# Performance work log

Measured on AMD Instinct MI355X. Metric: run time of the kernel, lower is better.

The kernel has to match this reference:

```python
import jax, jax.numpy as jnp
import numpy as np
import math

EPS = 0.1
N_ITER = 200
SCALE = 1.0
ATOL = 1e-4
RTOL = 1e-4
THRESH = 100.0
D = 2
LOGZ = math.log((2.0 * math.pi * EPS) ** (D / 2.0))


def setup_inputs() -> dict:
    key = jax.random.key(0)
    k1, k2 = jax.random.split(key)
    n, m = 4096, 4096
    # points scaled so C/eps stays O(1) -> K well within fp32 range
    x_spt = 0.3 * jax.random.normal(k1, (n, D), dtype=jnp.float32)
    y_spt = 0.3 * jax.random.normal(k2, (m, D), dtype=jnp.float32)
    x_w = jnp.ones((n,), jnp.float32) / n
    y_w = jnp.ones((m,), jnp.float32) / m
    return {"x_w": x_w, "x_spt": x_spt, "y_w": y_w, "y_spt": y_spt}


def _cdist2(x, y):
    # squared euclidean distance matrix [n, m] via gemm form
    x2 = jnp.sum(x * x, axis=1)
    y2 = jnp.sum(y * y, axis=1)
    d2 = x2[:, None] + y2[None, :] - 2.0 * (x @ y.T)
    return jnp.maximum(d2, 0.0)


def _getK(C, x_w, y_w, a, b):
    return jnp.exp(-(C + a[:, None] + b[None, :]) / EPS - LOGZ) * x_w[:, None] * y_w[None, :]


def _sinkhorn(C, x_w, y_w):
    # balanced Sinkhorn fixed point with absorption/stabilization, mirrors torch loop
    n, m = C.shape
    u0 = jnp.ones((n,), C.dtype)
    v0 = jnp.ones((m,), C.dtype)
    a0 = jnp.zeros((n,), C.dtype)
    b0 = jnp.zeros((m,), C.dtype)
    K0 = _getK(C, x_w, y_w, a0, b0)
    yw_norm = jnp.max(jnp.abs(y_w))

    def cond(st):
        i, u, v, a, b, K, done = st
        return (i < N_ITER) & (~done)

    def body(st):
        i, u, v, a, b, K, done = st
        v = y_w / (K.T @ u)      # proxdiv_balanced
        u = x_w / (K @ v)
        err = jnp.max(jnp.abs(v * (K.T @ u) - y_w))
        done = (err < ATOL) | (err / yw_norm < RTOL)
        stab = (jnp.maximum(jnp.max(jnp.abs(u)), jnp.max(jnp.abs(v))) > THRESH) & (~done)

        def do_stab(ops):
            u_, v_, a_, b_, K_ = ops
            a2 = a_ - EPS * jnp.log(u_)
            b2 = b_ - EPS * jnp.log(v_)
            return (jnp.ones_like(u_), jnp.ones_like(v_), a2, b2, _getK(C, x_w, y_w, a2, b2))

        u, v, a, b, K = jax.lax.cond(stab, do_stab, lambda ops: ops, (u, v, a, b, K))
        return (i + 1, u, v, a, b, K, done)

    st = jax.lax.while_loop(cond, body, (jnp.int32(0), u0, v0, a0, b0, K0, jnp.bool_(False)))
    return st[1], st[2], st[3], st[4]


def _obj_dual(C, x_w, y_w, u, v, a, b):
    f = -EPS * jnp.log(u) + a
    g = -EPS * jnp.log(v) + b
    f_cts = EPS * jax.nn.logsumexp((-C - g[None, :]) / EPS + jnp.log(y_w)[None, :], axis=1) - EPS * LOGZ
    g_cts = EPS * jax.nn.logsumexp((-C - f[:, None]) / EPS + jnp.log(x_w)[:, None], axis=0) - EPS * LOGZ
    f1 = f_cts @ x_w   # F_indicator_star (balanced)
    f2 = g_cts @ y_w
    plan = jnp.exp(-(C + f_cts[:, None] + g_cts[None, :]) / EPS - LOGZ) * x_w[:, None] * y_w[None, :]
    return -f1 - f2 - EPS * jnp.sum(plan)


def reference(x_w, x_spt, y_w, y_spt):
    C = _cdist2(x_spt, y_spt) / (2.0 * SCALE ** 2)
    u, v, a, b = _sinkhorn(C, x_w, y_w)
    return _obj_dual(C, x_w, y_w, u, v, a, b)
```

## Files before the change

### kernel.cpp

```cpp
#include <hip/hip_runtime.h>
#include <math.h>

#define N 4096

static constexpr float F_EPS     = 0.1f;
static constexpr float F_EPSLOGZ = -0.046470802658470075f;
static constexpr float F_ATOL    = 1e-4f;
static constexpr float F_RTOL    = 1e-4f;
static constexpr int   NITER     = 200;
static constexpr int   NB        = 256;
static constexpr int   BT        = 256;
static constexpr float K2        = 14.426950408889634f;
static constexpr float HK2       = 7.213475204444817f;
static constexpr float C1        = -0.6704311637146724f;
static constexpr float LN2       = 0.6931471805599453f;
static constexpr unsigned SALT   = 0x40000000u;

__device__ __forceinline__ float wsum(float x) {
#pragma unroll
  for (int o = 32; o; o >>= 1) x += __shfl_xor(x, o, 64);
  return x;
}
__device__ __forceinline__ float wmax(float x) {
#pragma unroll
  for (int o = 32; o; o >>= 1) x = fmaxf(x, __shfl_xor(x, o, 64));
  return x;
}

__device__ __forceinline__ float aload(const float* p) {
  return __hip_atomic_load(p, __ATOMIC_RELAXED, __HIP_MEMORY_SCOPE_AGENT);
}
__device__ __forceinline__ void astore(float* p, float v) {
  __hip_atomic_store(p, v, __ATOMIC_RELAXED, __HIP_MEMORY_SCOPE_AGENT);
}
__device__ __forceinline__ unsigned uload(const unsigned* p) {
  return __hip_atomic_load(p, __ATOMIC_RELAXED, __HIP_MEMORY_SCOPE_AGENT);
}
__device__ __forceinline__ void ustore(unsigned* p, unsigned v) {
  __hip_atomic_store(p, v, __ATOMIC_RELAXED, __HIP_MEMORY_SCOPE_AGENT);
}

__device__ __forceinline__ int gbar(unsigned* __restrict__ sync, const float* __restrict__ berr,
                                    float* __restrict__ sred, int* __restrict__ sdone,
                                    int bid, int tid, int lane, int wib,
                                    unsigned tgt, int decide, float ywn) {
  asm volatile("s_waitcnt vmcnt(0)" ::: "memory");
  __syncthreads();
  if (tid == 0) ustore(&sync[bid << 2], SALT + tgt);
  if (bid == 0) {
    while (uload(&sync[tid << 2]) != SALT + tgt) __builtin_amdgcn_s_sleep(1);
    __syncthreads();
    unsigned rel = SALT + (tgt << 1);
    if (decide) {
      const float m = wmax(aload(&berr[tid]));
      if (lane == 0) sred[wib] = m;
      __syncthreads();
      const float err = fmaxf(fmaxf(sred[0], sred[1]), fmaxf(sred[2], sred[3]));
      if ((err < F_ATOL) || (err / ywn < F_RTOL)) rel |= 1u;
      __syncthreads();
    }
    if (tid < 16) ustore(&sync[1024 + (tid << 4)], rel);
  }
  if (tid == 0) {
    unsigned f;
    unsigned* flag = &sync[1024 + ((bid & 15) << 4)];
    while (((f = uload(flag)) & ~1u) != SALT + (tgt << 1)) __builtin_amdgcn_s_sleep(1);
    *sdone = (int)(f & 1u);
  }
  __syncthreads();
  return *sdone;
}

__global__ void __launch_bounds__(BT) fused_kernel(
    const float* __restrict__ xw, const float2* __restrict__ xs,
    const float* __restrict__ yw, const float2* __restrict__ ys,
    float* __restrict__ pcol, float* __restrict__ prow, float* __restrict__ psav,
    float* __restrict__ berr, float* __restrict__ fcg, float* __restrict__ gcg,
    float* __restrict__ part, float* __restrict__ out, unsigned* __restrict__ sync) {
  __shared__ __align__(16) float2 xk[N];
  __shared__ __align__(16) float2 yk[N];
  __shared__ __align__(16) float  P[N];
  __shared__ float ew[4];
  __shared__ float sred[4];
  __shared__ int   sdone;
  const int tid  = threadIdx.x, bid = blockIdx.x;
  const int lane = tid & 63,    wib = tid >> 6;
  const int c0   = bid * 16 + wib * 4;
  unsigned tgt = 0;

  float mv = 0.f;
  for (int k = tid; k < N; k += BT) {
    const float2 xp = xs[k];
    const float2 yp = ys[k];
    xk[k] = make_float2(K2 * xp.x, K2 * xp.y);
    yk[k] = make_float2(K2 * yp.x, K2 * yp.y);
    P[k]  = log2f(xw[k]) - HK2 * (xp.x * xp.x + xp.y * xp.y);
    mv = fmaxf(mv, fabsf(yw[k]));
  }
  mv = wmax(mv);
  if (lane == 0) ew[wib] = mv;
  __syncthreads();
  const float ywn = fmaxf(fmaxf(ew[0], ew[1]), fmaxf(ew[2], ew[3]));
  __syncthreads();

  float2 xr[4], yc[4];
  float l2xw[4], l2yw[4], ywc[4];
#pragma unroll
  for (int q = 0; q < 4; ++q) {
    xr[q] = xs[c0 + q];
    yc[q] = ys[c0 + q];
    l2xw[q] = log2f(xw[c0 + q]);
    l2yw[q] = log2f(yw[c0 + q]);
    ywc[q]  = yw[c0 + q];
  }

  float accPrev[4];
  {
    float a[4] = {0.f, 0.f, 0.f, 0.f};
#pragma unroll 8
    for (int t = 0; t < 64; ++t) {
      const int i = (t << 6) + lane;
      const float2 c = xk[i]; const float w = P[i];
#pragma unroll
      for (int q = 0; q < 4; ++q)
        a[q] += exp2f(fmaf(c.x, yc[q].x, fmaf(c.y, yc[q].y, w)));
    }
#pragma unroll
    for (int q = 0; q < 4; ++q) {
      a[q] = wsum(a[q]);
      accPrev[q] = a[q];
      if (lane == 0) astore(&prow[c0 + q], l2yw[q] - log2f(a[q]));
    }
  }
  tgt++; gbar(sync, berr, sred, &sdone, bid, tid, lane, wib, tgt, 0, ywn);

  int converged = 0;
  for (int it = 0; it < NITER && !converged; ++it) {
    {
      float tmp[16];
#pragma unroll
      for (int q = 0; q < 16; ++q) tmp[q] = aload(&prow[tid + (q << 8)]);
#pragma unroll
      for (int q = 0; q < 16; ++q) P[tid + (q << 8)] = tmp[q];
    }
    __syncthreads();
    if (tid < 16) astore(&psav[(bid << 4) + tid], P[(bid << 4) + tid]);
    {
      float a[4] = {0.f, 0.f, 0.f, 0.f};
#pragma unroll 8
      for (int t = 0; t < 64; ++t) {
        const int j = (t << 6) + lane;
        const float2 c = yk[j]; const float w = P[j];
#pragma unroll
        for (int q = 0; q < 4; ++q)
          a[q] += exp2f(fmaf(c.x, xr[q].x, fmaf(c.y, xr[q].y, w)));
      }
#pragma unroll
      for (int q = 0; q < 4; ++q) {
        a[q] = wsum(a[q]);
        if (lane == 0) astore(&pcol[c0 + q], l2xw[q] - log2f(a[q]));
      }
    }
    tgt++; gbar(sync, berr, sred, &sdone, bid, tid, lane, wib, tgt, 0, ywn);

    {
      float tmp[16];
#pragma unroll
      for (int q = 0; q < 16; ++q) tmp[q] = aload(&pcol[tid + (q << 8)]);
#pragma unroll
      for (int q = 0; q < 16; ++q) P[tid + (q << 8)] = tmp[q];
    }
    __syncthreads();
    {
      float a[4] = {0.f, 0.f, 0.f, 0.f};
#pragma unroll 8
      for (int t = 0; t < 64; ++t) {
        const int i = (t << 6) + lane;
        const float2 c = xk[i]; const float w = P[i];
#pragma unroll
        for (int q = 0; q < 4; ++q)
          a[q] += exp2f(fmaf(c.x, yc[q].x, fmaf(c.y, yc[q].y, w)));
      }
      float e = 0.f;
#pragma unroll
      for (int q = 0; q < 4; ++q) {
        a[q] = wsum(a[q]);
        e = fmaxf(e, ywc[q] * fabsf(a[q] / accPrev[q] - 1.0f));
        accPrev[q] = a[q];
        if (lane == 0) astore(&prow[c0 + q], l2yw[q] - log2f(a[q]));
      }
      if (lane == 0) ew[wib] = e;
    }
    __syncthreads();
    if (tid == 0) astore(&berr[bid], fmaxf(fmaxf(ew[0], ew[1]), fmaxf(ew[2], ew[3])));
    tgt++;
    converged = gbar(sync, berr, sred, &sdone, bid, tid, lane, wib, tgt, 1, ywn);
  }

  {
    const int half = bid >> 7;
    const int base = (bid & 127) * 32 + wib * 8;
    {
      float tmp[16];
      if (half == 0) {
#pragma unroll
        for (int q = 0; q < 16; ++q) tmp[q] = aload(&psav[tid + (q << 8)]) + C1;
      } else {
#pragma unroll
        for (int q = 0; q < 16; ++q) tmp[q] = aload(&pcol[tid + (q << 8)]);
      }
#pragma unroll
      for (int q = 0; q < 16; ++q) P[tid + (q << 8)] = tmp[q];
    }
    __syncthreads();
    float2 rc[8]; float sq2[8]; float acc[8];
#pragma unroll
    for (int q = 0; q < 8; ++q) {
      const int r = base + q;
      rc[q] = half ? ys[r] : xs[r];
      sq2[q] = rc[q].x * rc[q].x + rc[q].y * rc[q].y;
      acc[q] = 0.f;
    }
    if (half == 0) {
#pragma unroll 4
      for (int t = 0; t < 64; ++t) {
        const int j = (t << 6) + lane;
        const float2 c = yk[j]; const float w = P[j];
#pragma unroll
        for (int q = 0; q < 8; ++q)
          acc[q] += exp2f(fmaf(c.x, rc[q].x, fmaf(c.y, rc[q].y, w)));
      }
    } else {
#pragma unroll 4
      for (int t = 0; t < 64; ++t) {
        const int i = (t << 6) + lane;
        const float2 c = xk[i]; const float w = P[i];
#pragma unroll
        for (int q = 0; q < 8; ++q)
          acc[q] += exp2f(fmaf(c.x, rc[q].x, fmaf(c.y, rc[q].y, w)));
      }
    }
#pragma unroll
    for (int q = 0; q < 8; ++q) acc[q] = wsum(acc[q]);
    if (lane == 0) {
#pragma unroll
      for (int q = 0; q < 8; ++q) {
        const int r = base + q;
        const float val = F_EPS * fmaf(LN2, log2f(acc[q]), -5.f * sq2[q]) - F_EPSLOGZ;
        astore(half ? &gcg[r] : &fcg[r], val);
      }
    }
  }
  tgt++; gbar(sync, berr, sred, &sdone, bid, tid, lane, wib, tgt, 0, ywn);

  {
    {
      float tmp[16];
#pragma unroll
      for (int q = 0; q < 16; ++q) tmp[q] = aload(&gcg[tid + (q << 8)]);
#pragma unroll
      for (int q = 0; q < 16; ++q) {
        const int k = tid + (q << 8);
        const float2 yp = ys[k];
        const float y2k = yp.x * yp.x + yp.y * yp.y;
        P[k] = fmaf(-HK2, y2k, fmaf(-K2, tmp[q], log2f(yw[k]))) - C1;
      }
    }
    __syncthreads();
    float a[4], wx[4];
#pragma unroll
    for (int q = 0; q < 4; ++q) {
      const int r = c0 + q;
      const float x2r = xr[q].x * xr[q].x + xr[q].y * xr[q].y;
      wx[q] = fmaf(-HK2, x2r, fmaf(-K2, aload(&fcg[r]), l2xw[q]));
      a[q] = 0.f;
    }
#pragma unroll 8
    for (int t = 0; t < 64; ++t) {
      const int j = (t << 6) + lane;
      const float2 c = yk[j]; const float w = P[j];
#pragma unroll
      for (int q = 0; q < 4; ++q)
        a[q] += exp2f(fmaf(c.x, xr[q].x, fmaf(c.y, xr[q].y, w)));
    }
#pragma unroll
    for (int q = 0; q < 4; ++q) a[q] = wsum(a[q]);
    if (lane == 0)
      ew[wib] = ((exp2f(wx[0]) * a[0] + exp2f(wx[1]) * a[1]) +
                 (exp2f(wx[2]) * a[2] + exp2f(wx[3]) * a[3]));
    __syncthreads();
    if (tid == 0) astore(&part[bid], (ew[0] + ew[1]) + (ew[2] + ew[3]));
  }
  tgt++; gbar(sync, berr, sred, &sdone, bid, tid, lane, wib, tgt, 0, ywn);

  if (bid == 0) {
    float a1 = 0.f, a2 = 0.f;
    for (int i = tid; i < N; i += BT) {
      a1 += aload(&fcg[i]) * xw[i];
      a2 += aload(&gcg[i]) * yw[i];
    }
    const float a3 = aload(&part[tid]);
    float* r1 = P; float* r2 = P + 256; float* r3 = P + 512;
    r1[tid] = a1; r2[tid] = a2; r3[tid] = a3; __syncthreads();
    for (int s2 = 128; s2; s2 >>= 1) {
      if (tid < s2) { r1[tid] += r1[tid + s2]; r2[tid] += r2[tid + s2]; r3[tid] += r3[tid + s2]; }
      __syncthreads();
    }
    if (tid == 0) out[0] = -r1[0] - r2[0] - F_EPS * r3[0];
  }
}

extern "C" void kernel_launch(void* const* d_in, const int* in_sizes, int n_in,
                              void* d_out, int out_size, void* d_ws, size_t ws_size,
                              hipStream_t stream) {
  const float*  xw  = (const float*)d_in[0];
  const float2* xs2 = (const float2*)d_in[1];
  const float*  yw  = (const float*)d_in[2];
  const float2* ys2 = (const float2*)d_in[3];
  float* out = (float*)d_out;

  float* w = (float*)d_ws;
  float *pcol = w,          *prow = w + 4096,  *psav = w + 8192,
        *fcg  = w + 12288,  *gcg  = w + 16384,
        *berr = w + 20480,  *part = w + 20736;
  unsigned* sync = (unsigned*)(w + 20992);

  fused_kernel<<<NB, BT, 0, stream>>>(xw, xs2, yw, ys2,
                                      pcol, prow, psav, berr, fcg, gcg, part, out, sync);
}
```

Baseline: 139.5 us.

## Replace centralized grid barrier with all-to-all slot barrier carrying payloads

Replaces the two-level grid barrier, where block 0 gathers arrivals and then broadcasts a release flag, with a double-buffered slot array. Every block writes its arrival tag together with a float payload, and every thread polls one slot, so the error max-reduction and the final partial sums travel with the barrier itself. This removes one round trip per barrier and drops the final barrier, since the last reduction now waits only on block 0. Global exchanges of row and column potentials switch to 64-bit packed atomic loads and stores. The cost is that all 256 threads of every block now poll global memory, raising memory traffic during spins.

Result: slower. 143.3 us (+2.7%).

```diff
diff --git a/kernel.cpp b/kernel.cpp
--- a/kernel.cpp
+++ b/kernel.cpp
@@ -16,6 +16,8 @@
 static constexpr float LN2       = 0.6931471805599453f;
 static constexpr unsigned SALT   = 0x40000000u;
 
+typedef unsigned long long u64;
+
 __device__ __forceinline__ float wsum(float x) {
 #pragma unroll
   for (int o = 32; o; o >>= 1) x += __shfl_xor(x, o, 64);
@@ -30,59 +32,49 @@
 __device__ __forceinline__ float aload(const float* p) {
   return __hip_atomic_load(p, __ATOMIC_RELAXED, __HIP_MEMORY_SCOPE_AGENT);
 }
-__device__ __forceinline__ void astore(float* p, float v) {
+__device__ __forceinline__ u64 uload64(const u64* p) {
+  return __hip_atomic_load(p, __ATOMIC_RELAXED, __HIP_MEMORY_SCOPE_AGENT);
+}
+__device__ __forceinline__ void ustore64(u64* p, u64 v) {
   __hip_atomic_store(p, v, __ATOMIC_RELAXED, __HIP_MEMORY_SCOPE_AGENT);
 }
-__device__ __forceinline__ unsigned uload(const unsigned* p) {
-  return __hip_atomic_load(p, __ATOMIC_RELAXED, __HIP_MEMORY_SCOPE_AGENT);
-}
-__device__ __forceinline__ void ustore(unsigned* p, unsigned v) {
-  __hip_atomic_store(p, v, __ATOMIC_RELAXED, __HIP_MEMORY_SCOPE_AGENT);
-}
-
-__device__ __forceinline__ int gbar(unsigned* __restrict__ sync, const float* __restrict__ berr,
-                                    float* __restrict__ sred, int* __restrict__ sdone,
-                                    int bid, int tid, int lane, int wib,
-                                    unsigned tgt, int decide, float ywn) {
+__device__ __forceinline__ u64 pack2(float lo, float hi) {
+  return ((u64)__float_as_uint(hi) << 32) | (u64)__float_as_uint(lo);
+}
+
+__device__ __forceinline__ float gbar(u64* __restrict__ slots01, float* __restrict__ red,
+                                      int bid, int tid, int lane, int wib,
+                                      unsigned tgt, float payload, int decide) {
+  u64* slots = slots01 + ((tgt & 1u) << 11);
   asm volatile("s_waitcnt vmcnt(0)" ::: "memory");
   __syncthreads();
-  if (tid == 0) ustore(&sync[bid << 2], SALT + tgt);
-  if (bid == 0) {
-    while (uload(&sync[tid << 2]) != SALT + tgt) __builtin_amdgcn_s_sleep(1);
-    __syncthreads();
-    unsigned rel = SALT + (tgt << 1);
-    if (decide) {
-      const float m = wmax(aload(&berr[tid]));
-      if (lane == 0) sred[wib] = m;
-      __syncthreads();
-      const float err = fmaxf(fmaxf(sred[0], sred[1]), fmaxf(sred[2], sred[3]));
-      if ((err < F_ATOL) || (err / ywn < F_RTOL)) rel |= 1u;
-      __syncthreads();
-    }
-    if (tid < 16) ustore(&sync[1024 + (tid << 4)], rel);
-  }
-  if (tid == 0) {
-    unsigned f;
-    unsigned* flag = &sync[1024 + ((bid & 15) << 4)];
-    while (((f = uload(flag)) & ~1u) != SALT + (tgt << 1)) __builtin_amdgcn_s_sleep(1);
-    *sdone = (int)(f & 1u);
+  if (tid == 0) ustore64(slots + ((u64)bid << 3), ((u64)__float_as_uint(payload) << 32) | (SALT + tgt));
+  u64 w;
+  while ((unsigned)(w = uload64(slots + ((u64)tid << 3))) != SALT + tgt)
+    __builtin_amdgcn_s_sleep(1);
+  if (decide) {
+    const float m = wmax(__uint_as_float((unsigned)(w >> 32)));
+    if (lane == 0) red[wib] = m;
+    __syncthreads();
+    const float r = fmaxf(fmaxf(red[0], red[1]), fmaxf(red[2], red[3]));
+    __syncthreads();
+    return r;
   }
   __syncthreads();
-  return *sdone;
+  return 0.f;
 }
 
 __global__ void __launch_bounds__(BT) fused_kernel(
     const float* __restrict__ xw, const float2* __restrict__ xs,
     const float* __restrict__ yw, const float2* __restrict__ ys,
     float* __restrict__ pcol, float* __restrict__ prow, float* __restrict__ psav,
-    float* __restrict__ berr, float* __restrict__ fcg, float* __restrict__ gcg,
-    float* __restrict__ part, float* __restrict__ out, unsigned* __restrict__ sync) {
+    float* __restrict__ fcg, float* __restrict__ gcg,
+    float* __restrict__ out, u64* __restrict__ slots) {
   __shared__ __align__(16) float2 xk[N];
   __shared__ __align__(16) float2 yk[N];
   __shared__ __align__(16) float  P[N];
   __shared__ float ew[4];
-  __shared__ float sred[4];
-  __shared__ int   sdone;
+  __shared__ float red[4];
   const int tid  = threadIdx.x, bid = blockIdx.x;
   const int lane = tid & 63,    wib = tid >> 6;
   const int c0   = bid * 16 + wib * 4;
@@ -125,26 +117,34 @@
       for (int q = 0; q < 4; ++q)
         a[q] += exp2f(fmaf(c.x, yc[q].x, fmaf(c.y, yc[q].y, w)));
     }
+    float o[4];
 #pragma unroll
     for (int q = 0; q < 4; ++q) {
       a[q] = wsum(a[q]);
       accPrev[q] = a[q];
-      if (lane == 0) astore(&prow[c0 + q], l2yw[q] - log2f(a[q]));
-    }
-  }
-  tgt++; gbar(sync, berr, sred, &sdone, bid, tid, lane, wib, tgt, 0, ywn);
+      o[q] = l2yw[q] - log2f(a[q]);
+    }
+    if (lane == 0) {
+      ustore64((u64*)&prow[c0],     pack2(o[0], o[1]));
+      ustore64((u64*)&prow[c0 + 2], pack2(o[2], o[3]));
+    }
+  }
+  tgt++; gbar(slots, red, bid, tid, lane, wib, tgt, 0.f, 0);
 
   int converged = 0;
   for (int it = 0; it < NITER && !converged; ++it) {
-    {
-      float tmp[16];
-#pragma unroll
-      for (int q = 0; q < 16; ++q) tmp[q] = aload(&prow[tid + (q << 8)]);
-#pragma unroll
-      for (int q = 0; q < 16; ++q) P[tid + (q << 8)] = tmp[q];
-    }
-    __syncthreads();
-    if (tid < 16) astore(&psav[(bid << 4) + tid], P[(bid << 4) + tid]);
+#pragma unroll
+    for (int q = 0; q < 8; ++q) {
+      const int idx = (tid << 1) + (q << 9);
+      const u64 d = uload64((const u64*)&prow[idx]);
+      P[idx]     = __uint_as_float((unsigned)d);
+      P[idx + 1] = __uint_as_float((unsigned)(d >> 32));
+    }
+    __syncthreads();
+    if (tid < 8) {
+      const int ix = (bid << 4) + (tid << 1);
+      ustore64((u64*)&psav[ix], pack2(P[ix], P[ix + 1]));
+    }
     {
       float a[4] = {0.f, 0.f, 0.f, 0.f};
 #pragma unroll 8
@@ -155,20 +155,25 @@
         for (int q = 0; q < 4; ++q)
           a[q] += exp2f(fmaf(c.x, xr[q].x, fmaf(c.y, xr[q].y, w)));
       }
+      float o[4];
 #pragma unroll
       for (int q = 0; q < 4; ++q) {
         a[q] = wsum(a[q]);
-        if (lane == 0) astore(&pcol[c0 + q], l2xw[q] - log2f(a[q]));
-      }
-    }
-    tgt++; gbar(sync, berr, sred, &sdone, bid, tid, lane, wib, tgt, 0, ywn);
-
-    {
-      float tmp[16];
-#pragma unroll
-      for (int q = 0; q < 16; ++q) tmp[q] = aload(&pcol[tid + (q << 8)]);
-#pragma unroll
-      for (int q = 0; q < 16; ++q) P[tid + (q << 8)] = tmp[q];
+        o[q] = l2xw[q] - log2f(a[q]);
+      }
+      if (lane == 0) {
+        ustore64((u64*)&pcol[c0],     pack2(o[0], o[1]));
+        ustore64((u64*)&pcol[c0 + 2], pack2(o[2], o[3]));
+      }
+    }
+    tgt++; gbar(slots, red, bid, tid, lane, wib, tgt, 0.f, 0);
+
+#pragma unroll
+    for (int q = 0; q < 8; ++q) {
+      const int idx = (tid << 1) + (q << 9);
+      const u64 d = uload64((const u64*)&pcol[idx]);
+      P[idx]     = __uint_as_float((unsigned)d);
+      P[idx + 1] = __uint_as_float((unsigned)(d >> 32));
     }
     __syncthreads();
     {
@@ -181,44 +186,53 @@
         for (int q = 0; q < 4; ++q)
           a[q] += exp2f(fmaf(c.x, yc[q].x, fmaf(c.y, yc[q].y, w)));
       }
-      float e = 0.f;
+      float e = 0.f, o[4];
 #pragma unroll
       for (int q = 0; q < 4; ++q) {
         a[q] = wsum(a[q]);
         e = fmaxf(e, ywc[q] * fabsf(a[q] / accPrev[q] - 1.0f));
         accPrev[q] = a[q];
-        if (lane == 0) astore(&prow[c0 + q], l2yw[q] - log2f(a[q]));
-      }
-      if (lane == 0) ew[wib] = e;
-    }
-    __syncthreads();
-    if (tid == 0) astore(&berr[bid], fmaxf(fmaxf(ew[0], ew[1]), fmaxf(ew[2], ew[3])));
+        o[q] = l2yw[q] - log2f(a[q]);
+      }
+      if (lane == 0) {
+        ustore64((u64*)&prow[c0],     pack2(o[0], o[1]));
+        ustore64((u64*)&prow[c0 + 2], pack2(o[2], o[3]));
+        ew[wib] = e;
+      }
+    }
+    __syncthreads();
+    const float blkerr = fmaxf(fmaxf(ew[0], ew[1]), fmaxf(ew[2], ew[3]));
     tgt++;
-    converged = gbar(sync, berr, sred, &sdone, bid, tid, lane, wib, tgt, 1, ywn);
-  }
-
+    const float err = gbar(slots, red, bid, tid, lane, wib, tgt, blkerr, 1);
+    converged = (err < F_ATOL) || (err / ywn < F_RTOL);
+  }
+
+  float sa12;
   {
     const int half = bid >> 7;
     const int base = (bid & 127) * 32 + wib * 8;
-    {
-      float tmp[16];
+#pragma unroll
+    for (int q = 0; q < 8; ++q) {
+      const int idx = (tid << 1) + (q << 9);
+      u64 d;
       if (half == 0) {
-#pragma unroll
-        for (int q = 0; q < 16; ++q) tmp[q] = aload(&psav[tid + (q << 8)]) + C1;
+        d = uload64((const u64*)&psav[idx]);
+        P[idx]     = __uint_as_float((unsigned)d) + C1;
+        P[idx + 1] = __uint_as_float((unsigned)(d >> 32)) + C1;
       } else {
-#pragma unroll
-        for (int q = 0; q < 16; ++q) tmp[q] = aload(&pcol[tid + (q << 8)]);
-      }
-#pragma unroll
-      for (int q = 0; q < 16; ++q) P[tid + (q << 8)] = tmp[q];
-    }
-    __syncthreads();
-    float2 rc[8]; float sq2[8]; float acc[8];
+        d = uload64((const u64*)&pcol[idx]);
+        P[idx]     = __uint_as_float((unsigned)d);
+        P[idx + 1] = __uint_as_float((unsigned)(d >> 32));
+      }
+    }
+    __syncthreads();
+    float2 rc[8]; float sq2[8]; float acc[8]; float wq[8];
 #pragma unroll
     for (int q = 0; q < 8; ++q) {
       const int r = base + q;
       rc[q] = half ? ys[r] : xs[r];
       sq2[q] = rc[q].x * rc[q].x + rc[q].y * rc[q].y;
+      wq[q] = half ? yw[r] : xw[r];
       acc[q] = 0.f;
     }
     if (half == 0) {
@@ -242,29 +256,34 @@
     }
 #pragma unroll
     for (int q = 0; q < 8; ++q) acc[q] = wsum(acc[q]);
+    float vals[8]; float s = 0.f;
+#pragma unroll
+    for (int q = 0; q < 8; ++q) {
+      vals[q] = F_EPS * fmaf(LN2, log2f(acc[q]), -5.f * sq2[q]) - F_EPSLOGZ;
+      s += vals[q] * wq[q];
+    }
     if (lane == 0) {
-#pragma unroll
-      for (int q = 0; q < 8; ++q) {
-        const int r = base + q;
-        const float val = F_EPS * fmaf(LN2, log2f(acc[q]), -5.f * sq2[q]) - F_EPSLOGZ;
-        astore(half ? &gcg[r] : &fcg[r], val);
-      }
-    }
-  }
-  tgt++; gbar(sync, berr, sred, &sdone, bid, tid, lane, wib, tgt, 0, ywn);
+      float* dst = half ? gcg : fcg;
+#pragma unroll
+      for (int q = 0; q < 4; ++q)
+        ustore64((u64*)&dst[base + (q << 1)], pack2(vals[q << 1], vals[(q << 1) + 1]));
+      red[wib] = s;
+    }
+    __syncthreads();
+    sa12 = (red[0] + red[1]) + (red[2] + red[3]);
+  }
+  tgt++; gbar(slots, red, bid, tid, lane, wib, tgt, 0.f, 0);
 
   {
-    {
-      float tmp[16];
-#pragma unroll
-      for (int q = 0; q < 16; ++q) tmp[q] = aload(&gcg[tid + (q << 8)]);
-#pragma unroll
-      for (int q = 0; q < 16; ++q) {
-        const int k = tid + (q << 8);
-        const float2 yp = ys[k];
-        const float y2k = yp.x * yp.x + yp.y * yp.y;
-        P[k] = fmaf(-HK2, y2k, fmaf(-K2, tmp[q], log2f(yw[k]))) - C1;
-      }
+#pragma unroll
+    for (int q = 0; q < 8; ++q) {
+      const int idx = (tid << 1) + (q << 9);
+      const u64 d = uload64((const u64*)&gcg[idx]);
+      const float g0 = __uint_as_float((unsigned)d);
+      const float g1 = __uint_as_float((unsigned)(d >> 32));
+      const float2 y0 = ys[idx], y1 = ys[idx + 1];
+      P[idx]     = fmaf(-HK2, y0.x * y0.x + y0.y * y0.y, fmaf(-K2, g0, log2f(yw[idx]))) - C1;
+      P[idx + 1] = fmaf(-HK2, y1.x * y1.x + y1.y * y1.y, fmaf(-K2, g1, log2f(yw[idx + 1]))) - C1;
     }
     __syncthreads();
     float a[4], wx[4];
@@ -289,24 +308,25 @@
       ew[wib] = ((exp2f(wx[0]) * a[0] + exp2f(wx[1]) * a[1]) +
                  (exp2f(wx[2]) * a[2] + exp2f(wx[3]) * a[3]));
     __syncthreads();
-    if (tid == 0) astore(&part[bid], (ew[0] + ew[1]) + (ew[2] + ew[3]));
-  }
-  tgt++; gbar(sync, berr, sred, &sdone, bid, tid, lane, wib, tgt, 0, ywn);
-
-  if (bid == 0) {
-    float a1 = 0.f, a2 = 0.f;
-    for (int i = tid; i < N; i += BT) {
-      a1 += aload(&fcg[i]) * xw[i];
-      a2 += aload(&gcg[i]) * yw[i];
-    }
-    const float a3 = aload(&part[tid]);
-    float* r1 = P; float* r2 = P + 256; float* r3 = P + 512;
-    r1[tid] = a1; r2[tid] = a2; r3[tid] = a3; __syncthreads();
+    const float partb = (ew[0] + ew[1]) + (ew[2] + ew[3]);
+    const float pay = sa12 + F_EPS * partb;
+
+    tgt++;
+    u64* fsl = slots + ((tgt & 1u) << 11);
+    asm volatile("s_waitcnt vmcnt(0)" ::: "memory");
+    __syncthreads();
+    if (tid == 0) ustore64(fsl + ((u64)bid << 3), ((u64)__float_as_uint(pay) << 32) | (SALT + tgt));
+    if (bid != 0) return;
+    u64 w2;
+    while ((unsigned)(w2 = uload64(fsl + ((u64)tid << 3))) != SALT + tgt)
+      __builtin_amdgcn_s_sleep(1);
+    P[tid] = __uint_as_float((unsigned)(w2 >> 32));
+    __syncthreads();
     for (int s2 = 128; s2; s2 >>= 1) {
-      if (tid < s2) { r1[tid] += r1[tid + s2]; r2[tid] += r2[tid + s2]; r3[tid] += r3[tid + s2]; }
+      if (tid < s2) P[tid] += P[tid + s2];
       __syncthreads();
     }
-    if (tid == 0) out[0] = -r1[0] - r2[0] - F_EPS * r3[0];
+    if (tid == 0) out[0] = -P[0];
   }
 }
 
@@ -321,10 +341,9 @@
 
   float* w = (float*)d_ws;
   float *pcol = w,          *prow = w + 4096,  *psav = w + 8192,
-        *fcg  = w + 12288,  *gcg  = w + 16384,
-        *berr = w + 20480,  *part = w + 20736;
-  unsigned* sync = (unsigned*)(w + 20992);
+        *fcg  = w + 12288,  *gcg  = w + 16384;
+  u64* slots = (u64*)(w + 20480);
 
   fused_kernel<<<NB, BT, 0, stream>>>(xw, xs2, yw, ys2,
-                                      pcol, prow, psav, berr, fcg, gcg, part, out, sync);
-}
+                                      pcol, prow, psav, fcg, gcg, out, slots);
+}
```
